# Performance work log

Measured on AMD Instinct MI355X. Metric: run time of the kernel, lower is better.

Reference implementation:

```python
import jax, jax.numpy as jnp
import numpy as np

B, N, F_IN, F_OUT = 8, 2048, 128, 64
ALPHA = 0.2  # LeakyReLU negative slope
NEG_BIG = -9e15


def setup_inputs() -> dict:
    key = jax.random.key(0)
    k1, k2, k3, k4 = jax.random.split(key, 4)
    x = jax.random.normal(k1, (B, N, F_IN), dtype=jnp.float32)
    adj = jax.random.randint(k2, (B, N, N), 0, 2, dtype=jnp.int32)
    # xavier-uniform-ish init scale for faithfulness (gain=1.414)
    w_lim = 1.414 * np.sqrt(6.0 / (F_IN + F_OUT))
    a_lim = 1.414 * np.sqrt(6.0 / (2 * F_OUT + 1))
    weight = jax.random.uniform(k3, (F_IN, F_OUT), minval=-w_lim, maxval=w_lim, dtype=jnp.float32)
    weight2 = jax.random.uniform(k4, (2 * F_OUT, 1), minval=-a_lim, maxval=a_lim, dtype=jnp.float32)
    return {"x": x, "adj": adj, "weight": weight, "weight2": weight2}


def reference(x, adj, weight, weight2):
    # Linear projection: [B, N, F_out]
    wh = jnp.einsum("bnf,fo->bno", x, weight)
    # Additive GAT decomposition of concat-score:
    # e_ij = leakyrelu(a1 . Wh_i + a2 . Wh_j)  == original concat @ weight2
    a1 = weight2[:F_OUT, 0]   # [F_out]
    a2 = weight2[F_OUT:, 0]   # [F_out]
    s1 = wh @ a1              # [B, N]
    s2 = wh @ a2              # [B, N]
    e = s1[:, :, None] + s2[:, None, :]          # [B, N, N]
    e = jnp.where(e > 0, e, ALPHA * e)            # LeakyReLU
    e = jnp.where(adj > 0, e, NEG_BIG)            # mask non-edges
    attention = jax.nn.softmax(e, axis=2)         # [B, N, N]
    # dropout is identity in eval mode (training=False)
    out = jnp.einsum("bij,bjo->bio", attention, wh)  # [B, N, F_out]
    return jax.nn.elu(out)
```

## Files before the change

kernel.cpp:

```cpp
#include <hip/hip_runtime.h>
#include <cstdint>
#include <cstddef>

#define B_    8
#define N_    2048
#define FIN   128
#define FOUT  64
#define ALPHA 0.2f
#define LOG2E 1.4426950408889634f

typedef __attribute__((ext_vector_type(8))) _Float16 half8;
typedef __attribute__((ext_vector_type(4))) _Float16 half4;
typedef __attribute__((ext_vector_type(4))) float float4v;

__global__ __launch_bounds__(256) void k0_convW(
    const float* __restrict__ W, _Float16* __restrict__ WtG)
{
    int o = blockIdx.x * 256 + threadIdx.x;
    int f = o >> 7, k = o & 127;
    float v = W[k * FOUT + f];
    _Float16 hi = (_Float16)v;
    _Float16 lo = (_Float16)(v - (float)hi);
    WtG[o] = hi;
    WtG[FOUT * FIN + o] = lo;
}

__global__ __launch_bounds__(256, 2) void k1_wh(
    const float* __restrict__ x, const _Float16* __restrict__ WtG,
    const float* __restrict__ w2, _Float16* __restrict__ whT,
    float* __restrict__ s1, float* __restrict__ s2)
{
    __shared__ __attribute__((aligned(16))) _Float16 xth[32][136];
    __shared__ __attribute__((aligned(16))) _Float16 xtl[32][136];
    __shared__ float s1p[4][32];
    __shared__ float s2p[4][32];

    int t = threadIdx.x, lane = t & 63, w = t >> 6;
    int b = blockIdx.x >> 6;
    int r0 = (blockIdx.x & 63) << 5;
    const float* xb = x + ((size_t)b * N_ + r0) * FIN;

    #pragma unroll
    for (int j = 0; j < 4; ++j) {
        int idx = t + j * 256;
        int row = idx >> 5;
        int k0 = (idx & 31) * 4;
        float4 v = ((const float4*)xb)[idx];
        float vv[4] = {v.x, v.y, v.z, v.w};
        half4 h, l;
        #pragma unroll
        for (int e = 0; e < 4; ++e) {
            _Float16 hi = (_Float16)vv[e];
            h[e] = hi;
            l[e] = (_Float16)(vv[e] - (float)hi);
        }
        *(half4*)&xth[row][k0] = h;
        *(half4*)&xtl[row][k0] = l;
    }
    __syncthreads();

    int l15 = lane & 15, quad = lane >> 4;
    int f0 = w * 16;

    half8 bh[4], bl[4];
    const _Float16* wgh = WtG + (f0 + l15) * FIN + quad * 8;
    #pragma unroll
    for (int c = 0; c < 4; ++c) {
        bh[c] = *(const half8*)(wgh + c * 32);
        bl[c] = *(const half8*)(wgh + FOUT * FIN + c * 32);
    }
    float a1f = w2[f0 + l15], a2f = w2[FOUT + f0 + l15];

    #pragma unroll
    for (int rt = 0; rt < 2; ++rt) {
        float4v acc = {0.f, 0.f, 0.f, 0.f};
        #pragma unroll
        for (int c = 0; c < 4; ++c) {
            half8 ah = *(const half8*)&xth[rt * 16 + l15][c * 32 + quad * 8];
            half8 al = *(const half8*)&xtl[rt * 16 + l15][c * 32 + quad * 8];
            acc = __builtin_amdgcn_mfma_f32_16x16x32_f16(ah, bh[c], acc, 0, 0, 0);
            acc = __builtin_amdgcn_mfma_f32_16x16x32_f16(ah, bl[c], acc, 0, 0, 0);
            acc = __builtin_amdgcn_mfma_f32_16x16x32_f16(al, bh[c], acc, 0, 0, 0);
        }
        half4 hv;
        #pragma unroll
        for (int reg = 0; reg < 4; ++reg) hv[reg] = (_Float16)acc[reg];
        *(half4*)(whT + ((size_t)b * FOUT + f0 + l15) * N_ + r0 + rt * 16 + quad * 4) = hv;

        #pragma unroll
        for (int reg = 0; reg < 4; ++reg) {
            float v1 = acc[reg] * a1f;
            float v2 = acc[reg] * a2f;
            #pragma unroll
            for (int m = 1; m <= 8; m <<= 1) {
                v1 += __shfl_xor(v1, m);
                v2 += __shfl_xor(v2, m);
            }
            if (l15 == 0) {
                s1p[w][rt * 16 + quad * 4 + reg] = v1;
                s2p[w][rt * 16 + quad * 4 + reg] = v2;
            }
        }
    }
    __syncthreads();
    if (t < 32) {
        float v = s1p[0][t] + s1p[1][t] + s1p[2][t] + s1p[3][t];
        s1[(size_t)b * N_ + r0 + t] = v;
    } else if (t < 64) {
        int r = t - 32;
        float v = s2p[0][r] + s2p[1][r] + s2p[2][r] + s2p[3][r];
        s2[(size_t)b * N_ + r0 + r] = v;
    }
}

__global__ __launch_bounds__(256, 4) void k2_attn(
    const int* __restrict__ adj, const _Float16* __restrict__ whT,
    const float* __restrict__ s1, const float* __restrict__ s2,
    float* __restrict__ out)
{
    __shared__ __attribute__((aligned(16))) _Float16 pT[16][520];
    __shared__ float lL[16];
    __shared__ float smaxL[4];

    int t = threadIdx.x, lane = t & 63, w = t >> 6;
    int b = blockIdx.x >> 7;
    int i0 = (blockIdx.x & 127) << 4;

    const float4* s2v = (const float4*)(s2 + (size_t)b * N_);
    float4 ua_ = s2v[t], ub_ = s2v[t + 256];
    float vm = fmaxf(fmaxf(fmaxf(ua_.x, ua_.y), fmaxf(ua_.z, ua_.w)),
                     fmaxf(fmaxf(ub_.x, ub_.y), fmaxf(ub_.z, ub_.w)));
    #pragma unroll
    for (int m = 32; m >= 1; m >>= 1) vm = fmaxf(vm, __shfl_xor(vm, m));
    if (lane == 0) smaxL[w] = vm;
    __syncthreads();
    float s2max = fmaxf(fmaxf(smaxL[0], smaxL[1]), fmaxf(smaxL[2], smaxL[3]));

    int l15 = lane & 15, quad = lane >> 4;
    int f0 = w * 16;

    float c1[4], c2[4], lacc[4];
    #pragma unroll
    for (int rr = 0; rr < 4; ++rr) {
        float sv = s1[(size_t)b * N_ + i0 + w * 4 + rr];
        float mm = sv + s2max;
        float mh = fmaxf(mm, ALPHA * mm);
        c1[rr] = (sv - mh) * LOG2E;
        c2[rr] = (ALPHA * sv - mh) * LOG2E;
        lacc[rr] = 0.f;
    }

    float4v acc = {0.f, 0.f, 0.f, 0.f};
    const _Float16* wB = whT + ((size_t)b * FOUT + f0 + l15) * N_ + quad * 8;

    for (int jc = 0; jc < N_; jc += 512) {
        const float* s2c = s2 + (size_t)b * N_ + jc + lane * 8;
        float4 sa = *(const float4*)s2c;
        float4 sb = *(const float4*)(s2c + 4);
        float ss[8] = {sa.x, sa.y, sa.z, sa.w, sb.x, sb.y, sb.z, sb.w};
        float u[8], ual[8];
        #pragma unroll
        for (int e = 0; e < 8; ++e) {
            u[e] = ss[e] * LOG2E;
            ual[e] = u[e] * ALPHA;
        }

        #pragma unroll
        for (int rr = 0; rr < 4; ++rr) {
            int r = w * 4 + rr;
            const int* ap = adj + ((size_t)b * N_ + i0 + r) * N_ + jc + lane * 8;
            int4 aj0 = *(const int4*)ap;
            int4 aj1 = *(const int4*)(ap + 4);
            int aa[8] = {aj0.x, aj0.y, aj0.z, aj0.w, aj1.x, aj1.y, aj1.z, aj1.w};
            half8 pf;
            float ls = 0.f;
            #pragma unroll
            for (int e = 0; e < 8; ++e) {
                float t2 = fmaxf(c1[rr] + u[e], c2[rr] + ual[e]);
#if __has_builtin(__builtin_amdgcn_exp2f)
                float p = __builtin_amdgcn_exp2f(t2);
#else
                float p = exp2f(t2);
#endif
                p = (aa[e] > 0) ? p : 0.f;
                ls += p;
                pf[e] = (_Float16)p;
            }
            lacc[rr] += ls;
            *(half8*)&pT[r][lane * 8] = pf;
        }

        if (jc == N_ - 512) {
            #pragma unroll
            for (int rr = 0; rr < 4; ++rr) {
                float v = lacc[rr];
                #pragma unroll
                for (int m = 32; m >= 1; m >>= 1) v += __shfl_xor(v, m);
                if (lane == 0) lL[w * 4 + rr] = v;
            }
        }
        __syncthreads();

        const _Float16* wp = wB + jc;
        #pragma unroll
        for (int kk = 0; kk < 16; ++kk) {
            half8 af = *(const half8*)&pT[l15][kk * 32 + quad * 8];
            half8 bf = *(const half8*)(wp + kk * 32);
            acc = __builtin_amdgcn_mfma_f32_16x16x32_f16(af, bf, acc, 0, 0, 0);
        }
        __syncthreads();
    }

    #pragma unroll
    for (int reg = 0; reg < 4; ++reg) {
        int row = quad * 4 + reg;
        float val = acc[reg] / lL[row];
        val = (val > 0.f) ? val : (__expf(val) - 1.f);
        out[((size_t)b * N_ + i0 + row) * FOUT + f0 + l15] = val;
    }
}

extern "C" void kernel_launch(void* const* d_in, const int* in_sizes, int n_in,
                              void* d_out, int out_size, void* d_ws, size_t ws_size,
                              hipStream_t stream) {
    const float* x   = (const float*)d_in[0];
    const int*   adj = (const int*)d_in[1];
    const float* W   = (const float*)d_in[2];
    const float* w2  = (const float*)d_in[3];
    float* out = (float*)d_out;

    _Float16* whT = (_Float16*)d_ws;
    float* s1 = (float*)((char*)d_ws + (size_t)B_ * FOUT * N_ * 2);
    float* s2 = s1 + (size_t)B_ * N_;
    _Float16* WtG = (_Float16*)(s2 + (size_t)B_ * N_);

    k0_convW<<<32, 256, 0, stream>>>(W, WtG);
    k1_wh<<<(B_ * N_) / 32, 256, 0, stream>>>(x, WtG, w2, whT, s1, s2);
    k2_attn<<<(B_ * N_) / 16, 256, 0, stream>>>(adj, whT, s1, s2, out);
}
```

Measured before the change: 219.7 us.

## Warp-specialize attention kernel into producer and MFMA consumer warps with double-buffered tiles

Doubles the block size to 512 threads. Four warps compute masked exp probabilities and prefetch adjacency and s2 into registers one chunk ahead; the other four warps run the MFMA accumulation. A double-buffered LDS tile lets the probability computation for the next 256-column chunk overlap with the matrix multiply on the current one, and the consumer warps get raised priority. The aim is to hide global load latency and serialization between the exp and MFMA phases, at the cost of fewer warps issuing memory loads and higher register pressure per block.

```diff
diff --git a/kernel.cpp b/kernel.cpp
--- a/kernel.cpp
+++ b/kernel.cpp
@@ -113,110 +113,159 @@
     }
 }
 
-__global__ __launch_bounds__(256, 4) void k2_attn(
+__global__ __launch_bounds__(512, 4) void k2_attn(
     const int* __restrict__ adj, const _Float16* __restrict__ whT,
     const float* __restrict__ s1, const float* __restrict__ s2,
     float* __restrict__ out)
 {
-    __shared__ __attribute__((aligned(16))) _Float16 pT[16][520];
+    __shared__ __attribute__((aligned(16))) _Float16 pT[2][16][264];
     __shared__ float lL[16];
-    __shared__ float smaxL[4];
+    __shared__ float smaxL[8];
 
     int t = threadIdx.x, lane = t & 63, w = t >> 6;
     int b = blockIdx.x >> 7;
     int i0 = (blockIdx.x & 127) << 4;
 
     const float4* s2v = (const float4*)(s2 + (size_t)b * N_);
-    float4 ua_ = s2v[t], ub_ = s2v[t + 256];
-    float vm = fmaxf(fmaxf(fmaxf(ua_.x, ua_.y), fmaxf(ua_.z, ua_.w)),
-                     fmaxf(fmaxf(ub_.x, ub_.y), fmaxf(ub_.z, ub_.w)));
+    float4 uv = s2v[t];
+    float vm = fmaxf(fmaxf(uv.x, uv.y), fmaxf(uv.z, uv.w));
     #pragma unroll
     for (int m = 32; m >= 1; m >>= 1) vm = fmaxf(vm, __shfl_xor(vm, m));
     if (lane == 0) smaxL[w] = vm;
     __syncthreads();
-    float s2max = fmaxf(fmaxf(smaxL[0], smaxL[1]), fmaxf(smaxL[2], smaxL[3]));
 
     int l15 = lane & 15, quad = lane >> 4;
-    int f0 = w * 16;
-
-    float c1[4], c2[4], lacc[4];
-    #pragma unroll
-    for (int rr = 0; rr < 4; ++rr) {
-        float sv = s1[(size_t)b * N_ + i0 + w * 4 + rr];
-        float mm = sv + s2max;
-        float mh = fmaxf(mm, ALPHA * mm);
-        c1[rr] = (sv - mh) * LOG2E;
-        c2[rr] = (ALPHA * sv - mh) * LOG2E;
-        lacc[rr] = 0.f;
-    }
-
-    float4v acc = {0.f, 0.f, 0.f, 0.f};
-    const _Float16* wB = whT + ((size_t)b * FOUT + f0 + l15) * N_ + quad * 8;
-
-    for (int jc = 0; jc < N_; jc += 512) {
-        const float* s2c = s2 + (size_t)b * N_ + jc + lane * 8;
-        float4 sa = *(const float4*)s2c;
-        float4 sb = *(const float4*)(s2c + 4);
-        float ss[8] = {sa.x, sa.y, sa.z, sa.w, sb.x, sb.y, sb.z, sb.w};
-        float u[8], ual[8];
-        #pragma unroll
-        for (int e = 0; e < 8; ++e) {
-            u[e] = ss[e] * LOG2E;
-            ual[e] = u[e] * ALPHA;
-        }
-
+
+    if (w < 4) {
+        float s2max = smaxL[0];
+        #pragma unroll
+        for (int i = 1; i < 8; ++i) s2max = fmaxf(s2max, smaxL[i]);
+
+        float c1[4], c2[4], lacc[4];
         #pragma unroll
         for (int rr = 0; rr < 4; ++rr) {
-            int r = w * 4 + rr;
-            const int* ap = adj + ((size_t)b * N_ + i0 + r) * N_ + jc + lane * 8;
-            int4 aj0 = *(const int4*)ap;
-            int4 aj1 = *(const int4*)(ap + 4);
-            int aa[8] = {aj0.x, aj0.y, aj0.z, aj0.w, aj1.x, aj1.y, aj1.z, aj1.w};
-            half8 pf;
-            float ls = 0.f;
-            #pragma unroll
-            for (int e = 0; e < 8; ++e) {
-                float t2 = fmaxf(c1[rr] + u[e], c2[rr] + ual[e]);
+            float sv = s1[(size_t)b * N_ + i0 + w * 4 + rr];
+            float mm = sv + s2max;
+            float mh = fmaxf(mm, ALPHA * mm);
+            c1[rr] = (sv - mh) * LOG2E;
+            c2[rr] = (ALPHA * sv - mh) * LOG2E;
+            lacc[rr] = 0.f;
+        }
+
+        const int* adjB = adj + ((size_t)b * N_ + i0 + w * 4) * N_ + lane * 4;
+        const float* s2B = s2 + (size_t)b * N_ + lane * 4;
+
+        int4  Ab[2][4];
+        float4 Sb[2];
+
+        #pragma unroll
+        for (int j = 0; j < 2; ++j) {
+            Sb[j] = *(const float4*)(s2B + j * 256);
+            #pragma unroll
+            for (int rr = 0; rr < 4; ++rr)
+                Ab[j][rr] = *(const int4*)(adjB + (size_t)rr * N_ + j * 256);
+        }
+
+        {
+            float4 sv = Sb[0];
+            float u[4]  = {sv.x * LOG2E, sv.y * LOG2E, sv.z * LOG2E, sv.w * LOG2E};
+            float ua[4] = {u[0] * ALPHA, u[1] * ALPHA, u[2] * ALPHA, u[3] * ALPHA};
+            #pragma unroll
+            for (int rr = 0; rr < 4; ++rr) {
+                int aa[4] = {Ab[0][rr].x, Ab[0][rr].y, Ab[0][rr].z, Ab[0][rr].w};
+                half4 pf;
+                float ls = 0.f;
+                #pragma unroll
+                for (int e = 0; e < 4; ++e) {
+                    float tt = fmaxf(c1[rr] + u[e], c2[rr] + ua[e]);
 #if __has_builtin(__builtin_amdgcn_exp2f)
-                float p = __builtin_amdgcn_exp2f(t2);
+                    float p = __builtin_amdgcn_exp2f(tt);
 #else
-                float p = exp2f(t2);
+                    float p = exp2f(tt);
 #endif
-                p = (aa[e] > 0) ? p : 0.f;
-                ls += p;
-                pf[e] = (_Float16)p;
-            }
-            lacc[rr] += ls;
-            *(half8*)&pT[r][lane * 8] = pf;
-        }
-
-        if (jc == N_ - 512) {
-            #pragma unroll
-            for (int rr = 0; rr < 4; ++rr) {
-                float v = lacc[rr];
+                    p = (aa[e] > 0) ? p : 0.f;
+                    ls += p;
+                    pf[e] = (_Float16)p;
+                }
+                lacc[rr] += ls;
+                *(half4*)&pT[0][w * 4 + rr][lane * 4] = pf;
+            }
+        }
+        __syncthreads();
+
+        #pragma unroll
+        for (int c = 0; c < 8; ++c) {
+            if (c < 6) {
+                Sb[c & 1] = *(const float4*)(s2B + (c + 2) * 256);
                 #pragma unroll
-                for (int m = 32; m >= 1; m >>= 1) v += __shfl_xor(v, m);
-                if (lane == 0) lL[w * 4 + rr] = v;
-            }
-        }
+                for (int rr = 0; rr < 4; ++rr)
+                    Ab[c & 1][rr] = *(const int4*)(adjB + (size_t)rr * N_ + (c + 2) * 256);
+            }
+            if (c < 7) {
+                float4 sv = Sb[(c + 1) & 1];
+                float u[4]  = {sv.x * LOG2E, sv.y * LOG2E, sv.z * LOG2E, sv.w * LOG2E};
+                float ua[4] = {u[0] * ALPHA, u[1] * ALPHA, u[2] * ALPHA, u[3] * ALPHA};
+                #pragma unroll
+                for (int rr = 0; rr < 4; ++rr) {
+                    int4 av = Ab[(c + 1) & 1][rr];
+                    int aa[4] = {av.x, av.y, av.z, av.w};
+                    half4 pf;
+                    float ls = 0.f;
+                    #pragma unroll
+                    for (int e = 0; e < 4; ++e) {
+                        float tt = fmaxf(c1[rr] + u[e], c2[rr] + ua[e]);
+#if __has_builtin(__builtin_amdgcn_exp2f)
+                        float p = __builtin_amdgcn_exp2f(tt);
+#else
+                        float p = exp2f(tt);
+#endif
+                        p = (aa[e] > 0) ? p : 0.f;
+                        ls += p;
+                        pf[e] = (_Float16)p;
+                    }
+                    lacc[rr] += ls;
+                    *(half4*)&pT[(c + 1) & 1][w * 4 + rr][lane * 4] = pf;
+                }
+                if (c == 6) {
+                    #pragma unroll
+                    for (int rr = 0; rr < 4; ++rr) {
+                        float v = lacc[rr];
+                        #pragma unroll
+                        for (int m = 32; m >= 1; m >>= 1) v += __shfl_xor(v, m);
+                        if (lane == 0) lL[w * 4 + rr] = v;
+                    }
+                }
+            }
+            __syncthreads();
+        }
+    } else {
+        int f0 = (w - 4) * 16;
+        float4v acc = {0.f, 0.f, 0.f, 0.f};
+        const _Float16* wB = whT + ((size_t)b * FOUT + f0 + l15) * N_ + quad * 8;
+
         __syncthreads();
 
-        const _Float16* wp = wB + jc;
-        #pragma unroll
-        for (int kk = 0; kk < 16; ++kk) {
-            half8 af = *(const half8*)&pT[l15][kk * 32 + quad * 8];
-            half8 bf = *(const half8*)(wp + kk * 32);
-            acc = __builtin_amdgcn_mfma_f32_16x16x32_f16(af, bf, acc, 0, 0, 0);
-        }
-        __syncthreads();
-    }
-
-    #pragma unroll
-    for (int reg = 0; reg < 4; ++reg) {
-        int row = quad * 4 + reg;
-        float val = acc[reg] / lL[row];
-        val = (val > 0.f) ? val : (__expf(val) - 1.f);
-        out[((size_t)b * N_ + i0 + row) * FOUT + f0 + l15] = val;
+        #pragma unroll
+        for (int c = 0; c < 8; ++c) {
+            const _Float16* wp = wB + c * 256;
+            __builtin_amdgcn_s_setprio(1);
+            #pragma unroll
+            for (int kk = 0; kk < 8; ++kk) {
+                half8 af = *(const half8*)&pT[c & 1][l15][kk * 32 + quad * 8];
+                half8 bf = *(const half8*)(wp + kk * 32);
+                acc = __builtin_amdgcn_mfma_f32_16x16x32_f16(af, bf, acc, 0, 0, 0);
+            }
+            __builtin_amdgcn_s_setprio(0);
+            __syncthreads();
+        }
+
+        #pragma unroll
+        for (int reg = 0; reg < 4; ++reg) {
+            int row = quad * 4 + reg;
+            float val = acc[reg] / lL[row];
+            val = (val > 0.f) ? val : (__expf(val) - 1.f);
+            out[((size_t)b * N_ + i0 + row) * FOUT + f0 + l15] = val;
+        }
     }
 }
 
@@ -236,5 +285,5 @@
 
     k0_convW<<<32, 256, 0, stream>>>(W, WtG);
     k1_wh<<<(B_ * N_) / 32, 256, 0, stream>>>(x, WtG, w2, whT, s1, s2);
-    k2_attn<<<(B_ * N_) / 16, 256, 0, stream>>>(adj, whT, s1, s2, out);
-}
+    k2_attn<<<(B_ * N_) / 16, 512, 0, stream>>>(adj, whT, s1, s2, out);
+}
```

Result: slower. 226.9 us (+3.3%).

## Double-buffer adjacency tiles into LDS via async global_load_lds in attention kernel

Applied to the files above, without the earlier changes.

The attention kernel now streams the int32 adjacency rows into a double-buffered LDS tile with global_load_lds, issuing the next chunk's loads before computing the current one. It also preloads the whT B-fragments into registers and drops one of the two barriers per iteration by double-buffering the probability tile. Chunks shrink from 512 to 256 columns and the loop is fully unrolled. The goal is to overlap adjacency memory traffic, the dominant byte stream, with the exp and MFMA work. In exchange it uses hand-set vmcnt waits that depend on exact instruction counts and risks extra register pressure.

```diff
diff --git a/kernel.cpp b/kernel.cpp
--- a/kernel.cpp
+++ b/kernel.cpp
@@ -118,7 +118,8 @@
     const float* __restrict__ s1, const float* __restrict__ s2,
     float* __restrict__ out)
 {
-    __shared__ __attribute__((aligned(16))) _Float16 pT[16][520];
+    __shared__ __attribute__((aligned(16))) int adjS[2][16][256];
+    __shared__ __attribute__((aligned(16))) _Float16 pT[2][16][264];
     __shared__ float lL[16];
     __shared__ float smaxL[4];
 
@@ -150,47 +151,71 @@
         lacc[rr] = 0.f;
     }
 
+    const int* adjL = adj + ((size_t)b * N_ + i0 + w * 4) * N_ + lane * 4;
+    const float* s2L = s2 + (size_t)b * N_ + lane * 4;
+    float4 Sb[2];
+
+#define STAGE(cn, bf) do {                                                   \
+        _Pragma("unroll")                                                    \
+        for (int rr = 0; rr < 4; ++rr) {                                     \
+            const int* src_ = adjL + (size_t)rr * N_ + (cn) * 256;           \
+            __builtin_amdgcn_global_load_lds(                                \
+                (const __attribute__((address_space(1))) void*)src_,         \
+                (__attribute__((address_space(3))) void*)&adjS[bf][w * 4 + rr][0], \
+                16, 0, 0);                                                   \
+        }                                                                    \
+        Sb[bf] = *(const float4*)(s2L + (cn) * 256);                         \
+    } while (0)
+
+    STAGE(0, 0);
+
     float4v acc = {0.f, 0.f, 0.f, 0.f};
     const _Float16* wB = whT + ((size_t)b * FOUT + f0 + l15) * N_ + quad * 8;
 
-    for (int jc = 0; jc < N_; jc += 512) {
-        const float* s2c = s2 + (size_t)b * N_ + jc + lane * 8;
-        float4 sa = *(const float4*)s2c;
-        float4 sb = *(const float4*)(s2c + 4);
-        float ss[8] = {sa.x, sa.y, sa.z, sa.w, sb.x, sb.y, sb.z, sb.w};
-        float u[8], ual[8];
-        #pragma unroll
-        for (int e = 0; e < 8; ++e) {
-            u[e] = ss[e] * LOG2E;
-            ual[e] = u[e] * ALPHA;
-        }
-
-        #pragma unroll
-        for (int rr = 0; rr < 4; ++rr) {
-            int r = w * 4 + rr;
-            const int* ap = adj + ((size_t)b * N_ + i0 + r) * N_ + jc + lane * 8;
-            int4 aj0 = *(const int4*)ap;
-            int4 aj1 = *(const int4*)(ap + 4);
-            int aa[8] = {aj0.x, aj0.y, aj0.z, aj0.w, aj1.x, aj1.y, aj1.z, aj1.w};
-            half8 pf;
-            float ls = 0.f;
+    #pragma unroll
+    for (int c = 0; c < 8; ++c) {
+        half8 bfr[8];
+        const _Float16* wp = wB + c * 256;
+        #pragma unroll
+        for (int kk = 0; kk < 8; ++kk) bfr[kk] = *(const half8*)(wp + kk * 32);
+
+        if (c < 7) {
+            STAGE(c + 1, (c + 1) & 1);
+            asm volatile("s_waitcnt vmcnt(13)" ::: "memory");
+        } else {
+            asm volatile("s_waitcnt vmcnt(8)" ::: "memory");
+        }
+        __builtin_amdgcn_sched_barrier(0);
+
+        {
+            float4 sv = Sb[c & 1];
+            float u[4]  = {sv.x * LOG2E, sv.y * LOG2E, sv.z * LOG2E, sv.w * LOG2E};
+            float ua[4] = {u[0] * ALPHA, u[1] * ALPHA, u[2] * ALPHA, u[3] * ALPHA};
             #pragma unroll
-            for (int e = 0; e < 8; ++e) {
-                float t2 = fmaxf(c1[rr] + u[e], c2[rr] + ual[e]);
+            for (int rr = 0; rr < 4; ++rr) {
+                int r = w * 4 + rr;
+                int4 av = *(const int4*)&adjS[c & 1][r][lane * 4];
+                int aa[4] = {av.x, av.y, av.z, av.w};
+                half4 pf;
+                float ls = 0.f;
+                #pragma unroll
+                for (int e = 0; e < 4; ++e) {
+                    float tt = fmaxf(c1[rr] + u[e], c2[rr] + ua[e]);
 #if __has_builtin(__builtin_amdgcn_exp2f)
-                float p = __builtin_amdgcn_exp2f(t2);
+                    float p = __builtin_amdgcn_exp2f(tt);
 #else
-                float p = exp2f(t2);
+                    float p = exp2f(tt);
 #endif
-                p = (aa[e] > 0) ? p : 0.f;
-                ls += p;
-                pf[e] = (_Float16)p;
-            }
-            lacc[rr] += ls;
-            *(half8*)&pT[r][lane * 8] = pf;
-        }
-
-        if (jc == N_ - 512) {
+                    p = (aa[e] > 0) ? p : 0.f;
+                    ls += p;
+                    pf[e] = (_Float16)p;
+                }
+                lacc[rr] += ls;
+                *(half4*)&pT[c & 1][r][lane * 4] = pf;
+            }
+        }
+
+        if (c == 7) {
             #pragma unroll
             for (int rr = 0; rr < 4; ++rr) {
                 float v = lacc[rr];
@@ -199,17 +224,16 @@
                 if (lane == 0) lL[w * 4 + rr] = v;
             }
         }
+
         __syncthreads();
 
-        const _Float16* wp = wB + jc;
-        #pragma unroll
-        for (int kk = 0; kk < 16; ++kk) {
-            half8 af = *(const half8*)&pT[l15][kk * 32 + quad * 8];
-            half8 bf = *(const half8*)(wp + kk * 32);
-            acc = __builtin_amdgcn_mfma_f32_16x16x32_f16(af, bf, acc, 0, 0, 0);
-        }
-        __syncthreads();
-    }
+        #pragma unroll
+        for (int kk = 0; kk < 8; ++kk) {
+            half8 af = *(const half8*)&pT[c & 1][l15][kk * 32 + quad * 8];
+            acc = __builtin_amdgcn_mfma_f32_16x16x32_f16(af, bfr[kk], acc, 0, 0, 0);
+        }
+    }
+#undef STAGE
 
     #pragma unroll
     for (int reg = 0; reg < 4; ++reg) {
```

Result: faster. 214.0 us (-2.6%).
